# Kernel optimization log

Measured on AMD Instinct MI355X. Metric: run time of the kernel, lower is better.

The kernel has to match this reference:

```python
import jax, jax.numpy as jnp
import numpy as np

# pywt 'db4' decomposition filters (8 taps)
DEC_LO = np.array([-0.010597401784997278, 0.032883011666982945, 0.030841381835986965,
                   -0.18703481171888114, -0.02798376941698385, 0.6308807679295904,
                   0.7148465705525415, 0.23037781330885523], dtype=np.float32)
DEC_HI = np.array([-0.23037781330885523, 0.7148465705525415, -0.6308807679295904,
                   -0.02798376941698385, 0.18703481171888114, 0.030841381835986965,
                   -0.032883011666982945, -0.010597401784997278], dtype=np.float32)
FLEN = 8


def _dwt_last_axis(x, kern):
    """Single-level DWT along the last axis, pywt 'symmetric' mode.
    Equivalent to: pad symmetric by FLEN-1, np.convolve(ext, filt, 'valid')[1::2].
    kern: [2, 1, FLEN] (already time-reversed filters -> cross-correlation == convolution).
    Returns (lo, hi) each of shape x.shape[:-1] + (floor((n+FLEN-1)/2),).
    """
    pad = [(0, 0)] * (x.ndim - 1) + [(FLEN - 1, FLEN - 1)]
    xp = jnp.pad(x, pad, mode='symmetric')[..., 1:]  # drop 1 -> stride-2 grid starts at offset 1
    lead = xp.shape[:-1]
    xr = xp.reshape(-1, 1, xp.shape[-1])             # [N, 1, Lp]
    y = jax.lax.conv_general_dilated(
        xr, kern, window_strides=(2,), padding='VALID',
        dimension_numbers=('NCH', 'OIH', 'NCH'))     # [N, 2, out]
    y = y.reshape(lead + (2, y.shape[-1]))
    return y[..., 0, :], y[..., 1, :]


def setup_inputs() -> dict:
    key = jax.random.key(0)
    x = jax.random.normal(key, (8, 32, 512, 512), dtype=jnp.float32)
    return {"x": x}


def reference(x):
    # Batched 2D db4 DWT (pywt.dwt2, mode='symmetric') over [B, C, H, W].
    kern = jnp.stack([jnp.asarray(DEC_LO)[::-1], jnp.asarray(DEC_HI)[::-1]])[:, None, :]  # [2,1,8]
    # filter along W (axis -1)
    a_w, d_w = _dwt_last_axis(x, kern)
    # filter along H (axis -2): swap H/W, filter last axis, swap back
    def along_h(t):
        lo, hi = _dwt_last_axis(jnp.swapaxes(t, -1, -2), kern)
        return jnp.swapaxes(lo, -1, -2), jnp.swapaxes(hi, -1, -2)
    LL, LH = along_h(a_w)   # LL = aa, LH = cH = 'da' (detail along H, approx along W)
    HL, HH = along_h(d_w)   # HL = cV = 'ad', HH = cD = 'dd'
    return jnp.stack([LL, LH, HL, HH])  # [4, B, C, Ho, Wo]
```

## Files before the change

kernel.cpp:

```cpp
#include <hip/hip_runtime.h>


namespace {

constexpr int N     = 512;
constexpr int HO    = 259;
constexpr int NBC   = 256;
constexpr int TOH   = 36;
constexpr int NB    = 8;
constexpr int NPAIR = (2 * TOH + 6) / 2;
constexpr int LROW  = 520;

__device__ constexpr float GL[8] = {
     0.23037781330885523f,  0.7148465705525415f,   0.6308807679295904f,
    -0.02798376941698385f, -0.18703481171888114f,  0.030841381835986965f,
     0.032883011666982945f,-0.010597401784997278f};
__device__ constexpr float GH[8] = {
    -0.010597401784997278f,-0.032883011666982945f, 0.030841381835986965f,
     0.18703481171888114f, -0.02798376941698385f, -0.6308807679295904f,
     0.7148465705525415f,  -0.23037781330885523f};

__device__ __forceinline__ int ext_row(int j) {
    int v = j - 7;
    v = (j < 7)     ? (6 - j)         : v;
    v = (j > N + 6) ? (2 * N + 6 - j) : v;
    return v;
}

typedef __attribute__((address_space(1))) const unsigned int ga_u32;
typedef __attribute__((address_space(3))) unsigned int       ls_u32;

__global__ __launch_bounds__(256)
void dwt2_db4_v13(const float* __restrict__ x, float* __restrict__ out) {
    __shared__ float ring[6][2][LROW];

    const int tid  = threadIdx.x;
    const int wv   = tid >> 6;
    const int lane = tid & 63;
    const int band = blockIdx.x & (NB - 1);
    const int bc   = blockIdx.x >> 3;
    const int ho0  = band * TOH;
    const int eh0  = 2 * ho0 + 1;
    const float* __restrict__ img = x + (size_t)bc * (N * N);
    float* __restrict__ ob = out + (size_t)bc * (HO * HO);
    const size_t sub = (size_t)NBC * HO * HO;
    const int c = tid;

    float Pll[4] = {0,0,0,0}, Plh[4] = {0,0,0,0};
    float Phl[4] = {0,0,0,0}, Phh[4] = {0,0,0,0};
    float Qll[4] = {0,0,0,0}, Qlh[4] = {0,0,0,0};
    float Qhl[4] = {0,0,0,0}, Qhh[4] = {0,0,0,0};
    float lo, hi, lo2 = 0.f, hi2 = 0.f;

#define STAGE(p_, slot_) do {                                                 \
    const int r_   = 2 * (p_) + (wv >> 1);                                    \
    const int src_ = ext_row(eh0 + r_);                                       \
    const float* g_ = img + (size_t)src_ * N + ((wv & 1) << 8) + (lane << 2); \
    float* l_ = &ring[slot_][wv >> 1][(wv & 1) << 8];                         \
    __builtin_amdgcn_global_load_lds((ga_u32*)g_, (ls_u32*)l_, 16, 0, 0);     \
} while (0)

#define STAGE3(p0_, s0_) do {                                                 \
    if ((p0_)     < NPAIR) STAGE((p0_),     (s0_));                           \
    if ((p0_) + 1 < NPAIR) STAGE((p0_) + 1, (s0_) + 1);                       \
    if ((p0_) + 2 < NPAIR) STAGE((p0_) + 2, (s0_) + 2);                       \
} while (0)

#define HROW(slot_, half_) do {                                               \
    const float* rp_ = &ring[slot_][half_][0];                                \
    lo = 0.f; hi = 0.f;                                                       \
    if (c >= 3) {                                                             \
        const int b_ = 2 * c - 6;                                             \
        _Pragma("unroll")                                                     \
        for (int f = 0; f < 8; ++f) {                                         \
            const float v_ = rp_[b_ + f];                                     \
            lo = fmaf(v_, GL[f], lo);  hi = fmaf(v_, GH[f], hi);              \
        }                                                                     \
    } else {                                                                  \
        _Pragma("unroll")                                                     \
        for (int f = 0; f < 8; ++f) {                                         \
            const int j_ = 2 * c + 1 + f;                                     \
            const float v_ = rp_[j_ < 7 ? 6 - j_ : j_ - 7];                   \
            lo = fmaf(v_, GL[f], lo);  hi = fmaf(v_, GH[f], hi);              \
        }                                                                     \
    }                                                                         \
    if (tid < 3) {                                                            \
        lo2 = 0.f; hi2 = 0.f;                                                 \
        _Pragma("unroll")                                                     \
        for (int f = 0; f < 8; ++f) {                                         \
            const int j_ = 513 + 2 * tid + f;                                 \
            const float v_ = rp_[j_ <= 518 ? j_ - 7 : 1030 - j_];             \
            lo2 = fmaf(v_, GL[f], lo2);  hi2 = fmaf(v_, GH[f], hi2);          \
        }                                                                     \
    }                                                                         \
} while (0)

#define UPDK(k_, s_) do {                                                     \
    Pll[s_] = fmaf(lo, GL[k_], Pll[s_]);  Plh[s_] = fmaf(lo, GH[k_], Plh[s_]);\
    Phl[s_] = fmaf(hi, GL[k_], Phl[s_]);  Phh[s_] = fmaf(hi, GH[k_], Phh[s_]);\
} while (0)

#define UPDQ(k_, s_) do {                                                     \
    Qll[s_] = fmaf(lo2, GL[k_], Qll[s_]); Qlh[s_] = fmaf(lo2, GH[k_], Qlh[s_]);\
    Qhl[s_] = fmaf(hi2, GL[k_], Qhl[s_]); Qhh[s_] = fmaf(hi2, GH[k_], Qhh[s_]);\
} while (0)

#define FIN(s_, uo_) do {                                                     \
    const int ho_ = ho0 + (uo_);                                              \
    if (ho_ < HO) {                                                           \
        const size_t p_ = (size_t)ho_ * HO + c;                               \
        ob[p_]           = Pll[s_];  ob[sub + p_]     = Plh[s_];              \
        ob[2 * sub + p_] = Phl[s_];  ob[3 * sub + p_] = Phh[s_];              \
        if (tid < 3) {                                                        \
            const size_t q_ = (size_t)ho_ * HO + 256 + tid;                   \
            ob[q_]           = Qll[s_];  ob[sub + q_]     = Qlh[s_];          \
            ob[2 * sub + q_] = Qhl[s_];  ob[3 * sub + q_] = Qhh[s_];          \
        }                                                                     \
    }                                                                         \
    Pll[s_] = 0.f; Plh[s_] = 0.f; Phl[s_] = 0.f; Phh[s_] = 0.f;               \
    Qll[s_] = 0.f; Qlh[s_] = 0.f; Qhl[s_] = 0.f; Qhh[s_] = 0.f;               \
} while (0)

#define PAIRF(sl_, ph_, uo_) do {                                             \
    HROW(sl_, 0);                                                             \
    UPDK(0, (3+(ph_))&3); UPDK(2, (2+(ph_))&3);                               \
    UPDK(4, (1+(ph_))&3); UPDK(6, (ph_)&3);                                   \
    if (tid < 3) { UPDQ(0, (3+(ph_))&3); UPDQ(2, (2+(ph_))&3);                \
                   UPDQ(4, (1+(ph_))&3); UPDQ(6, (ph_)&3); }                  \
    HROW(sl_, 1);                                                             \
    UPDK(1, (3+(ph_))&3); UPDK(3, (2+(ph_))&3);                               \
    UPDK(5, (1+(ph_))&3); UPDK(7, (ph_)&3);                                   \
    if (tid < 3) { UPDQ(1, (3+(ph_))&3); UPDQ(3, (2+(ph_))&3);                \
                   UPDQ(5, (1+(ph_))&3); UPDQ(7, (ph_)&3); }                  \
    FIN((ph_) & 3, uo_);                                                      \
} while (0)

    STAGE3(0, 0);
    __syncthreads();
    STAGE3(3, 3);
    HROW(0,0); UPDK(0,0);                       if (tid<3) { UPDQ(0,0); }
    HROW(0,1); UPDK(1,0);                       if (tid<3) { UPDQ(1,0); }
    HROW(1,0); UPDK(0,1); UPDK(2,0);            if (tid<3) { UPDQ(0,1); UPDQ(2,0); }
    HROW(1,1); UPDK(1,1); UPDK(3,0);            if (tid<3) { UPDQ(1,1); UPDQ(3,0); }
    HROW(2,0); UPDK(0,2); UPDK(2,1); UPDK(4,0); if (tid<3) { UPDQ(0,2); UPDQ(2,1); UPDQ(4,0); }
    HROW(2,1); UPDK(1,2); UPDK(3,1); UPDK(5,0); if (tid<3) { UPDQ(1,2); UPDQ(3,1); UPDQ(5,0); }
    __syncthreads();

    #pragma unroll 1
    for (int g = 0; g < 3; ++g) {
        const int pb = 12 * g;
        const int ub = 12 * g;
        STAGE3(pb + 6, 0);
        PAIRF(3, 0, ub + 0); PAIRF(4, 1, ub + 1); PAIRF(5, 2, ub + 2);
        __syncthreads();
        STAGE3(pb + 9, 3);
        PAIRF(0, 3, ub + 3); PAIRF(1, 0, ub + 4); PAIRF(2, 1, ub + 5);
        __syncthreads();
        STAGE3(pb + 12, 0);
        PAIRF(3, 2, ub + 6); PAIRF(4, 3, ub + 7); PAIRF(5, 0, ub + 8);
        __syncthreads();
        STAGE3(pb + 15, 3);
        PAIRF(0, 1, ub + 9); PAIRF(1, 2, ub + 10); PAIRF(2, 3, ub + 11);
        __syncthreads();
    }

#undef PAIRF
#undef FIN
#undef UPDQ
#undef UPDK
#undef HROW
#undef STAGE3
#undef STAGE
}

}

extern "C" void kernel_launch(void* const* d_in, const int* in_sizes, int n_in,
                              void* d_out, int out_size, void* d_ws, size_t ws_size,
                              hipStream_t stream) {
    const float* x = (const float*)d_in[0];
    float* out = (float*)d_out;
    dwt2_db4_v13<<<NB * NBC, 256, 0, stream>>>(x, out);
}
```

Before: 128.3 us.

## Offload boundary columns to a fifth wavefront and vectorize horizontal taps with float2 LDS reads

Adds a fifth wavefront per block that computes the symmetric-boundary output columns (the left three and right three), so the main four wavefronts run a branch-free interior path. Interior threads now read LDS as float2 pairs and compute both rows of a pair together, which drops the divergent tid<3 Q accumulators and the extra per-row boundary work. The cost is 25% more threads per block, mostly idle in the fifth wave. That wave still takes part in every barrier but issues no staging loads.

Result: faster. 125.3 us (-2.3%).

```diff
diff --git a/kernel.cpp b/kernel.cpp
--- a/kernel.cpp
+++ b/kernel.cpp
@@ -8,8 +8,10 @@
 constexpr int NBC   = 256;
 constexpr int TOH   = 36;
 constexpr int NB    = 8;
-constexpr int NPAIR = (2 * TOH + 6) / 2;
+constexpr int NPAIR = 39;
 constexpr int LROW  = 520;
+
+typedef float f2 __attribute__((ext_vector_type(2)));
 
 __device__ constexpr float GL[8] = {
      0.23037781330885523f,  0.7148465705525415f,   0.6308807679295904f,
@@ -30,13 +32,14 @@
 typedef __attribute__((address_space(1))) const unsigned int ga_u32;
 typedef __attribute__((address_space(3))) unsigned int       ls_u32;
 
-__global__ __launch_bounds__(256)
-void dwt2_db4_v13(const float* __restrict__ x, float* __restrict__ out) {
+__global__ __launch_bounds__(320)
+void dwt2_db4_v14(const float* __restrict__ x, float* __restrict__ out) {
     __shared__ float ring[6][2][LROW];
 
     const int tid  = threadIdx.x;
     const int wv   = tid >> 6;
     const int lane = tid & 63;
+    const bool w4  = (wv == 4);
     const int band = blockIdx.x & (NB - 1);
     const int bc   = blockIdx.x >> 3;
     const int ho0  = band * TOH;
@@ -44,13 +47,17 @@
     const float* __restrict__ img = x + (size_t)bc * (N * N);
     float* __restrict__ ob = out + (size_t)bc * (HO * HO);
     const size_t sub = (size_t)NBC * HO * HO;
-    const int c = tid;
+
+    const int  c      = tid;
+    const int  cb     = (c >= 3) ? (c - 3) : 0;
+    const int  lc     = (lane < 5) ? lane : 5;
+    const int  jb     = (lane < 3) ? (513 + 2 * lane) : (2 * lc - 5);
+    const int  colOut = w4 ? ((lane < 3) ? (256 + lane) : (lane - 3)) : c;
+    const bool valid  = w4 ? (lane < 6) : (c >= 3);
 
     float Pll[4] = {0,0,0,0}, Plh[4] = {0,0,0,0};
     float Phl[4] = {0,0,0,0}, Phh[4] = {0,0,0,0};
-    float Qll[4] = {0,0,0,0}, Qlh[4] = {0,0,0,0};
-    float Qhl[4] = {0,0,0,0}, Qhh[4] = {0,0,0,0};
-    float lo, hi, lo2 = 0.f, hi2 = 0.f;
+    float lo0, hi0, lo1, hi1;
 
 #define STAGE(p_, slot_) do {                                                 \
     const int r_   = 2 * (p_) + (wv >> 1);                                    \
@@ -66,109 +73,105 @@
     if ((p0_) + 2 < NPAIR) STAGE((p0_) + 2, (s0_) + 2);                       \
 } while (0)
 
-#define HROW(slot_, half_) do {                                               \
-    const float* rp_ = &ring[slot_][half_][0];                                \
-    lo = 0.f; hi = 0.f;                                                       \
-    if (c >= 3) {                                                             \
-        const int b_ = 2 * c - 6;                                             \
+#define HPAIR(sl_) do {                                                       \
+    if (!w4) {                                                                \
+        const f2* r0_ = (const f2*)&ring[sl_][0][0];                          \
+        const f2* r1_ = (const f2*)&ring[sl_][1][0];                          \
+        const f2 a0_ = r0_[cb], a1_ = r0_[cb+1], a2_ = r0_[cb+2], a3_ = r0_[cb+3]; \
+        const f2 b0_ = r1_[cb], b1_ = r1_[cb+1], b2_ = r1_[cb+2], b3_ = r1_[cb+3]; \
+        lo0 = a0_.x * GL[0];               hi0 = a0_.x * GH[0];               \
+        lo0 = fmaf(a0_.y, GL[1], lo0);     hi0 = fmaf(a0_.y, GH[1], hi0);     \
+        lo0 = fmaf(a1_.x, GL[2], lo0);     hi0 = fmaf(a1_.x, GH[2], hi0);     \
+        lo0 = fmaf(a1_.y, GL[3], lo0);     hi0 = fmaf(a1_.y, GH[3], hi0);     \
+        lo0 = fmaf(a2_.x, GL[4], lo0);     hi0 = fmaf(a2_.x, GH[4], hi0);     \
+        lo0 = fmaf(a2_.y, GL[5], lo0);     hi0 = fmaf(a2_.y, GH[5], hi0);     \
+        lo0 = fmaf(a3_.x, GL[6], lo0);     hi0 = fmaf(a3_.x, GH[6], hi0);     \
+        lo0 = fmaf(a3_.y, GL[7], lo0);     hi0 = fmaf(a3_.y, GH[7], hi0);     \
+        lo1 = b0_.x * GL[0];               hi1 = b0_.x * GH[0];               \
+        lo1 = fmaf(b0_.y, GL[1], lo1);     hi1 = fmaf(b0_.y, GH[1], hi1);     \
+        lo1 = fmaf(b1_.x, GL[2], lo1);     hi1 = fmaf(b1_.x, GH[2], hi1);     \
+        lo1 = fmaf(b1_.y, GL[3], lo1);     hi1 = fmaf(b1_.y, GH[3], hi1);     \
+        lo1 = fmaf(b2_.x, GL[4], lo1);     hi1 = fmaf(b2_.x, GH[4], hi1);     \
+        lo1 = fmaf(b2_.y, GL[5], lo1);     hi1 = fmaf(b2_.y, GH[5], hi1);     \
+        lo1 = fmaf(b3_.x, GL[6], lo1);     hi1 = fmaf(b3_.x, GH[6], hi1);     \
+        lo1 = fmaf(b3_.y, GL[7], lo1);     hi1 = fmaf(b3_.y, GH[7], hi1);     \
+    } else {                                                                  \
+        lo0 = 0.f; hi0 = 0.f; lo1 = 0.f; hi1 = 0.f;                           \
         _Pragma("unroll")                                                     \
         for (int f = 0; f < 8; ++f) {                                         \
-            const float v_ = rp_[b_ + f];                                     \
-            lo = fmaf(v_, GL[f], lo);  hi = fmaf(v_, GH[f], hi);              \
-        }                                                                     \
-    } else {                                                                  \
-        _Pragma("unroll")                                                     \
-        for (int f = 0; f < 8; ++f) {                                         \
-            const int j_ = 2 * c + 1 + f;                                     \
-            const float v_ = rp_[j_ < 7 ? 6 - j_ : j_ - 7];                   \
-            lo = fmaf(v_, GL[f], lo);  hi = fmaf(v_, GH[f], hi);              \
-        }                                                                     \
-    }                                                                         \
-    if (tid < 3) {                                                            \
-        lo2 = 0.f; hi2 = 0.f;                                                 \
-        _Pragma("unroll")                                                     \
-        for (int f = 0; f < 8; ++f) {                                         \
-            const int j_ = 513 + 2 * tid + f;                                 \
-            const float v_ = rp_[j_ <= 518 ? j_ - 7 : 1030 - j_];             \
-            lo2 = fmaf(v_, GL[f], lo2);  hi2 = fmaf(v_, GH[f], hi2);          \
+            const int j_   = jb + f;                                          \
+            const int idx_ = (j_ < 7) ? (6 - j_)                              \
+                           : ((j_ <= 518) ? (j_ - 7) : (1030 - j_));          \
+            const float v0_ = ring[sl_][0][idx_];                             \
+            const float v1_ = ring[sl_][1][idx_];                             \
+            lo0 = fmaf(v0_, GL[f], lo0);  hi0 = fmaf(v0_, GH[f], hi0);        \
+            lo1 = fmaf(v1_, GL[f], lo1);  hi1 = fmaf(v1_, GH[f], hi1);        \
         }                                                                     \
     }                                                                         \
 } while (0)
 
-#define UPDK(k_, s_) do {                                                     \
-    Pll[s_] = fmaf(lo, GL[k_], Pll[s_]);  Plh[s_] = fmaf(lo, GH[k_], Plh[s_]);\
-    Phl[s_] = fmaf(hi, GL[k_], Phl[s_]);  Phh[s_] = fmaf(hi, GH[k_], Phh[s_]);\
+#define UPDK0(k_, s_) do {                                                    \
+    Pll[s_] = fmaf(lo0, GL[k_], Pll[s_]); Plh[s_] = fmaf(lo0, GH[k_], Plh[s_]);\
+    Phl[s_] = fmaf(hi0, GL[k_], Phl[s_]); Phh[s_] = fmaf(hi0, GH[k_], Phh[s_]);\
 } while (0)
 
-#define UPDQ(k_, s_) do {                                                     \
-    Qll[s_] = fmaf(lo2, GL[k_], Qll[s_]); Qlh[s_] = fmaf(lo2, GH[k_], Qlh[s_]);\
-    Qhl[s_] = fmaf(hi2, GL[k_], Qhl[s_]); Qhh[s_] = fmaf(hi2, GH[k_], Qhh[s_]);\
+#define UPDK1(k_, s_) do {                                                    \
+    Pll[s_] = fmaf(lo1, GL[k_], Pll[s_]); Plh[s_] = fmaf(lo1, GH[k_], Plh[s_]);\
+    Phl[s_] = fmaf(hi1, GL[k_], Phl[s_]); Phh[s_] = fmaf(hi1, GH[k_], Phh[s_]);\
 } while (0)
 
 #define FIN(s_, uo_) do {                                                     \
     const int ho_ = ho0 + (uo_);                                              \
-    if (ho_ < HO) {                                                           \
-        const size_t p_ = (size_t)ho_ * HO + c;                               \
+    if (valid && ho_ < HO) {                                                  \
+        const size_t p_ = (size_t)ho_ * HO + colOut;                          \
         ob[p_]           = Pll[s_];  ob[sub + p_]     = Plh[s_];              \
         ob[2 * sub + p_] = Phl[s_];  ob[3 * sub + p_] = Phh[s_];              \
-        if (tid < 3) {                                                        \
-            const size_t q_ = (size_t)ho_ * HO + 256 + tid;                   \
-            ob[q_]           = Qll[s_];  ob[sub + q_]     = Qlh[s_];          \
-            ob[2 * sub + q_] = Qhl[s_];  ob[3 * sub + q_] = Qhh[s_];          \
-        }                                                                     \
     }                                                                         \
     Pll[s_] = 0.f; Plh[s_] = 0.f; Phl[s_] = 0.f; Phh[s_] = 0.f;               \
-    Qll[s_] = 0.f; Qlh[s_] = 0.f; Qhl[s_] = 0.f; Qhh[s_] = 0.f;               \
 } while (0)
 
 #define PAIRF(sl_, ph_, uo_) do {                                             \
-    HROW(sl_, 0);                                                             \
-    UPDK(0, (3+(ph_))&3); UPDK(2, (2+(ph_))&3);                               \
-    UPDK(4, (1+(ph_))&3); UPDK(6, (ph_)&3);                                   \
-    if (tid < 3) { UPDQ(0, (3+(ph_))&3); UPDQ(2, (2+(ph_))&3);                \
-                   UPDQ(4, (1+(ph_))&3); UPDQ(6, (ph_)&3); }                  \
-    HROW(sl_, 1);                                                             \
-    UPDK(1, (3+(ph_))&3); UPDK(3, (2+(ph_))&3);                               \
-    UPDK(5, (1+(ph_))&3); UPDK(7, (ph_)&3);                                   \
-    if (tid < 3) { UPDQ(1, (3+(ph_))&3); UPDQ(3, (2+(ph_))&3);                \
-                   UPDQ(5, (1+(ph_))&3); UPDQ(7, (ph_)&3); }                  \
+    HPAIR(sl_);                                                               \
+    UPDK0(0, (3+(ph_))&3); UPDK0(2, (2+(ph_))&3);                             \
+    UPDK0(4, (1+(ph_))&3); UPDK0(6, (ph_)&3);                                 \
+    UPDK1(1, (3+(ph_))&3); UPDK1(3, (2+(ph_))&3);                             \
+    UPDK1(5, (1+(ph_))&3); UPDK1(7, (ph_)&3);                                 \
     FIN((ph_) & 3, uo_);                                                      \
 } while (0)
 
-    STAGE3(0, 0);
+    if (!w4) STAGE3(0, 0);
     __syncthreads();
-    STAGE3(3, 3);
-    HROW(0,0); UPDK(0,0);                       if (tid<3) { UPDQ(0,0); }
-    HROW(0,1); UPDK(1,0);                       if (tid<3) { UPDQ(1,0); }
-    HROW(1,0); UPDK(0,1); UPDK(2,0);            if (tid<3) { UPDQ(0,1); UPDQ(2,0); }
-    HROW(1,1); UPDK(1,1); UPDK(3,0);            if (tid<3) { UPDQ(1,1); UPDQ(3,0); }
-    HROW(2,0); UPDK(0,2); UPDK(2,1); UPDK(4,0); if (tid<3) { UPDQ(0,2); UPDQ(2,1); UPDQ(4,0); }
-    HROW(2,1); UPDK(1,2); UPDK(3,1); UPDK(5,0); if (tid<3) { UPDQ(1,2); UPDQ(3,1); UPDQ(5,0); }
+    if (!w4) STAGE3(3, 3);
+    HPAIR(0); UPDK0(0,0);                       UPDK1(1,0);
+    HPAIR(1); UPDK0(0,1); UPDK0(2,0);           UPDK1(1,1); UPDK1(3,0);
+    HPAIR(2); UPDK0(0,2); UPDK0(2,1); UPDK0(4,0);
+              UPDK1(1,2); UPDK1(3,1); UPDK1(5,0);
     __syncthreads();
 
     #pragma unroll 1
     for (int g = 0; g < 3; ++g) {
         const int pb = 12 * g;
         const int ub = 12 * g;
-        STAGE3(pb + 6, 0);
+        STAGE_GROUP_1:;
+        if (!w4) STAGE3(pb + 6, 0);
         PAIRF(3, 0, ub + 0); PAIRF(4, 1, ub + 1); PAIRF(5, 2, ub + 2);
         __syncthreads();
-        STAGE3(pb + 9, 3);
+        if (!w4) STAGE3(pb + 9, 3);
         PAIRF(0, 3, ub + 3); PAIRF(1, 0, ub + 4); PAIRF(2, 1, ub + 5);
         __syncthreads();
-        STAGE3(pb + 12, 0);
+        if (!w4) STAGE3(pb + 12, 0);
         PAIRF(3, 2, ub + 6); PAIRF(4, 3, ub + 7); PAIRF(5, 0, ub + 8);
         __syncthreads();
-        STAGE3(pb + 15, 3);
+        if (!w4) STAGE3(pb + 15, 3);
         PAIRF(0, 1, ub + 9); PAIRF(1, 2, ub + 10); PAIRF(2, 3, ub + 11);
         __syncthreads();
     }
 
 #undef PAIRF
 #undef FIN
-#undef UPDQ
-#undef UPDK
-#undef HROW
+#undef UPDK1
+#undef UPDK0
+#undef HPAIR
 #undef STAGE3
 #undef STAGE
 }
@@ -180,5 +183,5 @@
                               hipStream_t stream) {
     const float* x = (const float*)d_in[0];
     float* out = (float*)d_out;
-    dwt2_db4_v13<<<NB * NBC, 256, 0, stream>>>(x, out);
+    dwt2_db4_v14<<<NB * NBC, 320, 0, stream>>>(x, out);
 }
```
